# Kernel optimization log

Hardware: AMD Instinct MI355X
Metric: run time of the kernel (lower is better)

## Reference

```python
import jax, jax.numpy as jnp
import numpy as np

MAX_SEQ_LEN = 256

def _membership(idx_list, seq_len):
    # idx_list: [B, K] int; returns [B, S] bool, True where position s (s>=1)
    # satisfies s-1 in idx_list (ignoring -1 padding and out-of-range entries).
    pos = jnp.arange(seq_len)  # [S]
    valid = (idx_list != -1) & (idx_list + 1 < seq_len)          # [B, K]
    hit = (pos[None, :, None] - 1) == idx_list[:, None, :]        # [B, S, K]
    return jnp.any(hit & valid[:, None, :], axis=-1)              # [B, S]

def setup_inputs() -> dict:
    key = jax.random.key(0)
    k1, k2, k3, k4, k5, k6 = jax.random.split(key, 6)
    B, S, H, K = 128, MAX_SEQ_LEN, 768, 64
    return {
        "bert_local_out": jax.random.normal(k1, (B, S, H), dtype=jnp.float32),
        "depend": jax.random.randint(k2, (B, K), 0, S),
        "depended": jax.random.randint(k3, (B, K), 0, S),
        "no_connect": jax.random.randint(k4, (B, K), 0, S),
        "depend_weight": jax.random.uniform(k5, (B,), dtype=jnp.float32),
        "depended_weight": jax.random.uniform(k6, (B,), dtype=jnp.float32),
    }

def reference(bert_local_out, depend, depended, no_connect,
              depend_weight, depended_weight):
    B, S, H = bert_local_out.shape
    pos = jnp.arange(S)

    # --- dependency_hidden: zero token j (j>=1) unless j-1 is in the list;
    # position 0 is always kept (loop starts at j=1). Padding -1 never matches.
    dep_mem_raw = jnp.any((pos[None, :, None] - 1) == depend[:, None, :] , axis=-1)
    dpd_mem_raw = jnp.any((pos[None, :, None] - 1) == depended[:, None, :], axis=-1)
    keep_dep = (pos[None, :] == 0) | dep_mem_raw            # [B, S]
    keep_dpd = (pos[None, :] == 0) | dpd_mem_raw
    depend_out = bert_local_out * keep_dep[:, :, None].astype(bert_local_out.dtype)
    depended_out = bert_local_out * keep_dpd[:, :, None].astype(bert_local_out.dtype)

    # --- weight_distrubute_local: start from zeros, copy pos 0, then scatter
    # depend_weight at depend+1, overwrite with depended_weight at depended+1,
    # then zero no_connect+1. Express as a per-position multiplier.
    dep_mem = _membership(depend, S)
    dpd_mem = _membership(depended, S)
    noc_mem = _membership(no_connect, S)
    zero = jnp.zeros((), bert_local_out.dtype)
    mult = jnp.where(dep_mem, depend_weight[:, None], zero)
    mult = jnp.where(dpd_mem, depended_weight[:, None], mult)
    mult = jnp.where(noc_mem, zero, mult)
    mult = jnp.where(pos[None, :] == 0, jnp.ones((), bert_local_out.dtype), mult)
    local_out2 = bert_local_out * mult[:, :, None]

    return depend_out, depended_out, local_out2
```

## Files before the change

### kernel.cpp

```cpp
#include <hip/hip_runtime.h>

#define SEQ 256
#define HID 768
#define KLEN 64
#define H4 (HID / 4)

__global__ __launch_bounds__(192) void dlcf_dca_fused(
    const float* __restrict__ x,
    const int*   __restrict__ depend,
    const int*   __restrict__ depended,
    const int*   __restrict__ no_connect,
    const float* __restrict__ dep_w,
    const float* __restrict__ dpd_w,
    float* __restrict__ out,
    size_t n4)
{
    const int r    = blockIdx.x;
    const int b    = r >> 8;
    const int s    = r & (SEQ - 1);
    const int lane = threadIdx.x & 63;
    const int target = s - 1;

    const int e_dep = depend[b * KLEN + lane];
    const int e_dpd = depended[b * KLEN + lane];
    const int e_noc = no_connect[b * KLEN + lane];

    const bool dep_raw = __any(e_dep == target);
    const bool dpd_raw = __any(e_dpd == target);

    const bool dep_mem = __any((e_dep == target) & (e_dep != -1) & (e_dep + 1 < SEQ));
    const bool dpd_mem = __any((e_dpd == target) & (e_dpd != -1) & (e_dpd + 1 < SEQ));
    const bool noc_mem = __any((e_noc == target) & (e_noc != -1) & (e_noc + 1 < SEQ));

    const float m0 = (s == 0 || dep_raw) ? 1.0f : 0.0f;
    const float m1 = (s == 0 || dpd_raw) ? 1.0f : 0.0f;

    float m2;
    if (s == 0)        m2 = 1.0f;
    else if (noc_mem)  m2 = 0.0f;
    else if (dpd_mem)  m2 = dpd_w[b];
    else if (dep_mem)  m2 = dep_w[b];
    else               m2 = 0.0f;

    const size_t base = (size_t)r * H4 + threadIdx.x;
    const float4* __restrict__ x4 = (const float4*)x;
    float4* __restrict__ o4 = (float4*)out;

    const float4 v = x4[base];
    o4[base]          = make_float4(v.x * m0, v.y * m0, v.z * m0, v.w * m0);
    o4[base + n4]     = make_float4(v.x * m1, v.y * m1, v.z * m1, v.w * m1);
    o4[base + 2 * n4] = make_float4(v.x * m2, v.y * m2, v.z * m2, v.w * m2);
}

extern "C" void kernel_launch(void* const* d_in, const int* in_sizes, int n_in,
                              void* d_out, int out_size, void* d_ws, size_t ws_size,
                              hipStream_t stream) {
    const float* x          = (const float*)d_in[0];
    const int*   depend     = (const int*)d_in[1];
    const int*   depended   = (const int*)d_in[2];
    const int*   no_connect = (const int*)d_in[3];
    const float* dep_w      = (const float*)d_in[4];
    const float* dpd_w      = (const float*)d_in[5];
    float* out = (float*)d_out;

    const int B = in_sizes[0] / (SEQ * HID);
    const size_t n4 = (size_t)in_sizes[0] / 4;

    dlcf_dca_fused<<<B * SEQ, 192, 0, stream>>>(
        x, depend, depended, no_connect, dep_w, dpd_w, out, n4);
}
```

Before: 365.5 us.

## Process several rows per wave with nontemporal loads and stores

```diff
diff --git a/kernel.cpp b/kernel.cpp
--- a/kernel.cpp
+++ b/kernel.cpp
@@ -4,68 +4,86 @@
 #define HID 768
 #define KLEN 64
 #define H4 (HID / 4)
+#define ROWS_PER_WAVE 4
+#define BLOCK 256
+#define WAVES_PER_BLOCK (BLOCK / 64)
 
-__global__ __launch_bounds__(192) void dlcf_dca_fused(
-    const float* __restrict__ x,
-    const int*   __restrict__ depend,
-    const int*   __restrict__ depended,
-    const int*   __restrict__ no_connect,
+typedef float f4 __attribute__((ext_vector_type(4)));
+
+__global__ __launch_bounds__(BLOCK) void dlcf_dca_fused(
+    const f4* __restrict__ x4,
+    const int* __restrict__ depend,
+    const int* __restrict__ depended,
+    const int* __restrict__ no_connect,
     const float* __restrict__ dep_w,
     const float* __restrict__ dpd_w,
-    float* __restrict__ out,
+    f4* __restrict__ o4,
     size_t n4)
 {
-    const int r    = blockIdx.x;
-    const int b    = r >> 8;
-    const int s    = r & (SEQ - 1);
-    const int lane = threadIdx.x & 63;
-    const int target = s - 1;
+    const int lane  = threadIdx.x & 63;
+    const int wid   = threadIdx.x >> 6;
+    const int chunk = blockIdx.x * WAVES_PER_BLOCK + wid;
+    const int row0  = chunk * ROWS_PER_WAVE;
+    const int b     = row0 >> 8;
 
     const int e_dep = depend[b * KLEN + lane];
     const int e_dpd = depended[b * KLEN + lane];
     const int e_noc = no_connect[b * KLEN + lane];
+    const bool dep_ok = (e_dep != -1) & (e_dep + 1 < SEQ);
+    const bool dpd_ok = (e_dpd != -1) & (e_dpd + 1 < SEQ);
+    const bool noc_ok = (e_noc != -1) & (e_noc + 1 < SEQ);
+    const float w1 = dep_w[b];
+    const float w2 = dpd_w[b];
 
-    const bool dep_raw = __any(e_dep == target);
-    const bool dpd_raw = __any(e_dpd == target);
+    #pragma unroll
+    for (int i = 0; i < ROWS_PER_WAVE; ++i) {
+        const int r = row0 + i;
+        const int s = r & (SEQ - 1);
+        const int t = s - 1;
 
-    const bool dep_mem = __any((e_dep == target) & (e_dep != -1) & (e_dep + 1 < SEQ));
-    const bool dpd_mem = __any((e_dpd == target) & (e_dpd != -1) & (e_dpd + 1 < SEQ));
-    const bool noc_mem = __any((e_noc == target) & (e_noc != -1) & (e_noc + 1 < SEQ));
+        const bool dep_raw = __any(e_dep == t);
+        const bool dpd_raw = __any(e_dpd == t);
+        const bool dep_mem = __any((e_dep == t) & dep_ok);
+        const bool dpd_mem = __any((e_dpd == t) & dpd_ok);
+        const bool noc_mem = __any((e_noc == t) & noc_ok);
 
-    const float m0 = (s == 0 || dep_raw) ? 1.0f : 0.0f;
-    const float m1 = (s == 0 || dpd_raw) ? 1.0f : 0.0f;
+        const float m0 = (s == 0 || dep_raw) ? 1.0f : 0.0f;
+        const float m1 = (s == 0 || dpd_raw) ? 1.0f : 0.0f;
+        float m2;
+        if (s == 0)        m2 = 1.0f;
+        else if (noc_mem)  m2 = 0.0f;
+        else if (dpd_mem)  m2 = w2;
+        else if (dep_mem)  m2 = w1;
+        else               m2 = 0.0f;
 
-    float m2;
-    if (s == 0)        m2 = 1.0f;
-    else if (noc_mem)  m2 = 0.0f;
-    else if (dpd_mem)  m2 = dpd_w[b];
-    else if (dep_mem)  m2 = dep_w[b];
-    else               m2 = 0.0f;
-
-    const size_t base = (size_t)r * H4 + threadIdx.x;
-    const float4* __restrict__ x4 = (const float4*)x;
-    float4* __restrict__ o4 = (float4*)out;
-
-    const float4 v = x4[base];
-    o4[base]          = make_float4(v.x * m0, v.y * m0, v.z * m0, v.w * m0);
-    o4[base + n4]     = make_float4(v.x * m1, v.y * m1, v.z * m1, v.w * m1);
-    o4[base + 2 * n4] = make_float4(v.x * m2, v.y * m2, v.z * m2, v.w * m2);
+        const size_t base = (size_t)r * H4 + lane;
+        #pragma unroll
+        for (int j = 0; j < H4 / 64; ++j) {
+            const size_t idx = base + (size_t)j * 64;
+            const f4 v = __builtin_nontemporal_load(&x4[idx]);
+            __builtin_nontemporal_store(v * m0, &o4[idx]);
+            __builtin_nontemporal_store(v * m1, &o4[idx + n4]);
+            __builtin_nontemporal_store(v * m2, &o4[idx + 2 * n4]);
+        }
+    }
 }
 
 extern "C" void kernel_launch(void* const* d_in, const int* in_sizes, int n_in,
                               void* d_out, int out_size, void* d_ws, size_t ws_size,
                               hipStream_t stream) {
-    const float* x          = (const float*)d_in[0];
+    const f4*    x4         = (const f4*)d_in[0];
     const int*   depend     = (const int*)d_in[1];
     const int*   depended   = (const int*)d_in[2];
     const int*   no_connect = (const int*)d_in[3];
     const float* dep_w      = (const float*)d_in[4];
     const float* dpd_w      = (const float*)d_in[5];
-    float* out = (float*)d_out;
+    f4* o4 = (f4*)d_out;
 
     const int B = in_sizes[0] / (SEQ * HID);
     const size_t n4 = (size_t)in_sizes[0] / 4;
+    const int rows = B * SEQ;
+    const int grid = rows / (ROWS_PER_WAVE * WAVES_PER_BLOCK);
 
-    dlcf_dca_fused<<<B * SEQ, 192, 0, stream>>>(
-        x, depend, depended, no_connect, dep_w, dpd_w, out, n4);
+    dlcf_dca_fused<<<grid, BLOCK, 0, stream>>>(
+        x4, depend, depended, no_connect, dep_w, dpd_w, o4, n4);
 }
```

After: 372.9 us. +2.0%, slower.
